# Kernel tuning notes

Hardware: AMD Instinct MI355X
Metric: run time of the kernel (lower is better)

Reference implementation:

```python
import jax, jax.numpy as jnp
import numpy as np
from jax import lax

G = 1000  # hard-coded grid size in ConvCNP.forward
LOG_2PI = float(np.log(2.0 * np.pi))


def _conv1d(x, w, b):
    # x: (B, Cin, L), w: (Cout, Cin, K), SAME padding, stride 1 (k=5, pad=2)
    y = lax.conv_general_dilated(x, w, (1,), 'SAME',
                                 dimension_numbers=('NCH', 'OIH', 'NCH'))
    return y + b[None, :, None]


def setup_inputs() -> dict:
    key = jax.random.key(0)
    ks = jax.random.split(key, 16)
    B, Nc, Nt = 32, 2048, 2048
    inp = {
        'x_context': jax.random.normal(ks[0], (B, 1, Nc), jnp.float32),
        'y_context': jax.random.normal(ks[1], (B, 1, Nc), jnp.float32),
        'x_target': jax.random.normal(ks[2], (B, 1, Nt), jnp.float32),
        'y_target': jax.random.normal(ks[3], (B, 1, Nt), jnp.float32),
        # learned kernel lengthscales (nn.Parameter init 0.5)
        'ls_x': jnp.asarray(0.5, jnp.float32),
        'ls_rho': jnp.asarray(0.5, jnp.float32),
        # SimpleCNN(2, 1): channels [2, 16, 32, 16, 2], k=5
        'W1': 0.1 * jax.random.normal(ks[4], (16, 2, 5), jnp.float32),
        'b1': jnp.zeros((16,), jnp.float32),
        'W2': 0.1 * jax.random.normal(ks[5], (32, 16, 5), jnp.float32),
        'b2': jnp.zeros((32,), jnp.float32),
        'W3': 0.1 * jax.random.normal(ks[6], (16, 32, 5), jnp.float32),
        'b3': jnp.zeros((16,), jnp.float32),
        'W4': 0.1 * jax.random.normal(ks[7], (2, 16, 5), jnp.float32),
        'b4': jnp.zeros((2,), jnp.float32),
    }
    return inp


def _forward(x_context, y_context, x_target, y_target,
             ls_x, ls_rho, W1, b1, W2, b2, W3, b3, W4, b4):
    B = x_context.shape[0]
    xc = x_context[:, 0, :]            # (B, Nc)
    xt = x_target[:, 0, :]             # (B, Nt)
    t = jnp.linspace(-2.2, 2.2, G).astype(x_context.dtype)  # (G,)

    # phi(y) = [1, y] density/signal channels: (B, 2, Nc)
    phi = jnp.concatenate([jnp.ones_like(y_context), y_context], axis=1)

    # EQ-kernel interpolation context -> grid: w[b,g,n] = exp(-(t_g-x_n)^2/(2 l^2))
    d2 = (t[None, :, None] - xc[:, None, :]) ** 2           # (B, G, Nc)
    w_x = jnp.exp(-d2 / (2.0 * ls_x * ls_x))
    h = jnp.einsum('bgn,bcn->bcg', w_x, phi)                # (B, 2, G)

    density = h[:, 0:1, :]
    rest = h[:, 1:, :] / (density + 1e-8)
    h = jnp.concatenate([density, rest], axis=1)            # (B, 2, G)

    # SimpleCNN
    y = jax.nn.relu(_conv1d(h, W1, b1))
    y = jax.nn.relu(_conv1d(y, W2, b2))
    y = jax.nn.relu(_conv1d(y, W3, b3))
    y = _conv1d(y, W4, b4)                                  # (B, 2, G)
    y_mu_grid = y[:, 0:1, :]
    y_sigma_grid = jax.nn.softplus(y[:, 1:2, :])
    y_grid = jnp.concatenate([y_mu_grid, y_sigma_grid], axis=1)  # (B, 2, G)

    # EQ-kernel interpolation grid -> targets
    d2t = (xt[:, :, None] - t[None, None, :]) ** 2          # (B, Nt, G)
    w_rho = jnp.exp(-d2t / (2.0 * ls_rho * ls_rho))
    y_pred = jnp.einsum('btg,bcg->bct', w_rho, y_grid)      # (B, 2, Nt)

    mu = y_pred[:, 0:1, :]
    sigma = y_pred[:, 1:2, :]

    # Normal(mu, sigma).log_prob(y_target), mean over points, sum over batch
    z = (y_target - mu) / sigma
    logp = -0.5 * z * z - jnp.log(sigma) - 0.5 * LOG_2PI    # (B, 1, Nt)
    loss = -jnp.sum(jnp.mean(logp, axis=-1))
    return mu.transpose(0, 2, 1), sigma.transpose(0, 2, 1), loss


def reference(x_context, y_context, x_target, y_target,
              ls_x, ls_rho, W1, b1, W2, b2, W3, b3, W4, b4):
    return _forward(x_context, y_context, x_target, y_target,
                    ls_x, ls_rho, W1, b1, W2, b2, W3, b3, W4, b4)
```

## Files before the change

### kernel.cpp

```cpp
#include <hip/hip_runtime.h>
#include <math.h>

#define G     1000
#define B     32
#define NC    2048
#define NT    2048
#define BN    (B * NT)
#define LOG2E 1.4426950408889634f
#define LN2PI 1.8378770664093453f

#if __has_builtin(__builtin_amdgcn_exp2f)
#define EXP2F(x) __builtin_amdgcn_exp2f(x)
#else
#define EXP2F(x) exp2f(x)
#endif

typedef float f32x2 __attribute__((ext_vector_type(2)));
#define PKFMA(a, b, c) __builtin_elementwise_fma(a, b, c)
#define SPLAT_LO(v)    __builtin_shufflevector(v, v, 0, 0)
#define SPLAT_HI(v)    __builtin_shufflevector(v, v, 1, 1)

__global__ __launch_bounds__(512) void k_smooth(
    const float* __restrict__ xc, const float* __restrict__ yc,
    const float* __restrict__ ls_x, float* __restrict__ h,
    float* __restrict__ loss_slot) {
  __shared__ float2 sxy[NC];
  __shared__ float2 part[8][64];
  if (blockIdx.x == 0 && blockIdx.y == 0 && threadIdx.x == 0) *loss_slot = 0.f;

  int tid = threadIdx.x;
  int b = blockIdx.y, tile = blockIdx.x;
  float ls  = ls_x[0];
  float s   = sqrtf(0.5f * LOG2E) / ls;
  float dlt = s * (4.4f / 999.f);

  const float* xb = xc + b * NC;
  const float* yb = yc + b * NC;
  for (int n = tid; n < NC; n += 512) sxy[n] = make_float2(s * xb[n], yb[n]);
  __syncthreads();

  int lane = tid & 63, w = tid >> 6;
  int ns = lane & 7, gr = lane >> 3;
  int g0 = tile * 64 + gr * 8;
  float v0 = s * -2.2f + dlt * (float)g0;
  float r  = EXP2F(-2.f * dlt * dlt);
  float r3 = r * r * r;
  float r4 = r3 * r;
  const f32x2 R4 = {r4, r4};

  f32x2 h0p[4], h1p[4];
  #pragma unroll
  for (int j = 0; j < 4; ++j) { h0p[j] = (f32x2)0.f; h1p[j] = (f32x2)0.f; }

  const float2* base = sxy + w * 256 + ns;
  #pragma unroll 4
  for (int i = 0; i < 32; ++i) {
    float2 v = base[i * 8];
    float a  = v.x - v0;
    float W0 = EXP2F(64.f - a * a);
    float q  = EXP2F(fmaf(2.f * dlt, a, -dlt * dlt));
    float qq = q * q;
    f32x2 W2 = {W0, W0 * q};
    f32x2 S2 = {qq * r, qq * r3};
    f32x2 y2 = {v.y, v.y};
    #pragma unroll
    for (int j = 0; j < 4; ++j) {
      h0p[j] += W2;
      h1p[j] = PKFMA(W2, y2, h1p[j]);
      W2 *= S2;
      S2 *= R4;
    }
  }
  #pragma unroll
  for (int m = 1; m < 8; m <<= 1) {
    #pragma unroll
    for (int j = 0; j < 4; ++j) {
      h0p[j].x += __shfl_xor(h0p[j].x, m);
      h0p[j].y += __shfl_xor(h0p[j].y, m);
      h1p[j].x += __shfl_xor(h1p[j].x, m);
      h1p[j].y += __shfl_xor(h1p[j].y, m);
    }
  }
  #pragma unroll
  for (int j = 0; j < 4; ++j) {
    if (ns == j) {
      part[w][gr * 8 + 2 * j]     = make_float2(h0p[j].x, h1p[j].x);
      part[w][gr * 8 + 2 * j + 1] = make_float2(h0p[j].y, h1p[j].y);
    }
  }
  __syncthreads();

  if (tid < 64) {
    int g = tile * 64 + tid;
    if (g < G) {
      float d0 = 0.f, d1 = 0.f;
      #pragma unroll
      for (int k = 0; k < 8; ++k) { float2 pv = part[k][tid]; d0 += pv.x; d1 += pv.y; }
      d0 *= 0x1p-64f;
      d1 *= 0x1p-64f;
      h[(b * 2 + 0) * G + g] = d0;
      h[(b * 2 + 1) * G + g] = d1 / (d0 + 1e-8f);
    }
  }
}

#define TILE  48
#define NTILE 21
#define CSTR  68

template <int CIN, int COUT, int S4>
__device__ __forceinline__ void conv8(
    const float* __restrict__ in, float* __restrict__ out,
    const float4* __restrict__ wf4, const float* __restrict__ w4p,
    const float* __restrict__ bias, int tid) {
  if (tid < COUT * 8) {
    int oc = tid % COUT;
    int i0 = (tid / COUT) * 8;
    float acc[8];
    float bb = bias[oc];
    #pragma unroll
    for (int p = 0; p < 8; ++p) acc[p] = bb;
    for (int ic = 0; ic < CIN; ++ic) {
      const float4* ip = (const float4*)(in + ic * CSTR + i0);
      float4 A = ip[0], Bv = ip[1], C = ip[2];
      float v[12] = {A.x, A.y, A.z, A.w, Bv.x, Bv.y, Bv.z, Bv.w, C.x, C.y, C.z, C.w};
      float4 w = wf4[oc * S4 + ic];
      float w4v = w4p[ic * COUT + oc];
      #pragma unroll
      for (int p = 0; p < 8; ++p)
        acc[p] = fmaf(v[p], w.x, fmaf(v[p+1], w.y, fmaf(v[p+2], w.z,
                 fmaf(v[p+3], w.w, fmaf(v[p+4], w4v, acc[p])))));
    }
    float* op = out + oc * CSTR + i0 + 2;
    #pragma unroll
    for (int j = 0; j < 4; ++j)
      *(float2*)(op + 2 * j) = make_float2(fmaxf(acc[2*j], 0.f), fmaxf(acc[2*j+1], 0.f));
  }
}

template <int CIN, int COUT, int S4>
__device__ __forceinline__ void conv4(
    const float* __restrict__ in, float* __restrict__ out,
    const float4* __restrict__ wf4, const float* __restrict__ w4p,
    const float* __restrict__ bias, int tid) {
  int oc = tid % COUT;
  int i0 = (tid / COUT) * 4;
  float acc[4];
  float bb = bias[oc];
  #pragma unroll
  for (int p = 0; p < 4; ++p) acc[p] = bb;
  for (int ic = 0; ic < CIN; ++ic) {
    const float4* ip = (const float4*)(in + ic * CSTR + i0);
    float4 A = ip[0], Bv = ip[1];
    float v[8] = {A.x, A.y, A.z, A.w, Bv.x, Bv.y, Bv.z, Bv.w};
    float4 w = wf4[oc * S4 + ic];
    float w4v = w4p[ic * COUT + oc];
    #pragma unroll
    for (int p = 0; p < 4; ++p)
      acc[p] = fmaf(v[p], w.x, fmaf(v[p+1], w.y, fmaf(v[p+2], w.z,
               fmaf(v[p+3], w.w, fmaf(v[p+4], w4v, acc[p])))));
  }
  float* op = out + oc * CSTR + i0 + 2;
  *(float2*)op       = make_float2(fmaxf(acc[0], 0.f), fmaxf(acc[1], 0.f));
  *(float2*)(op + 2) = make_float2(fmaxf(acc[2], 0.f), fmaxf(acc[3], 0.f));
}

__global__ __launch_bounds__(256, 2) void k_conv(
    const float* __restrict__ h,
    const float* __restrict__ W1, const float* __restrict__ Bs1,
    const float* __restrict__ W2, const float* __restrict__ Bs2,
    const float* __restrict__ W3, const float* __restrict__ Bs3,
    const float* __restrict__ W4, const float* __restrict__ Bs4,
    float* __restrict__ yg) {
  __shared__ __align__(16) float bufA[32 * CSTR], bufB[32 * CSTR];
  __shared__ float4 wf1[16 * 3], wf2[32 * 17], wf3[16 * 33];
  __shared__ float  w41[2 * 16], w42[16 * 32], w43[32 * 16];
  __shared__ float  wt4[162];
  __shared__ float  sB1[16], sB2[32], sB3[16], sB4[2];

  int tid  = threadIdx.x;
  int tile = blockIdx.x, b = blockIdx.y;
  int ts   = tile * TILE;

  if (tid < 32) {
    int oc = tid >> 1, ic = tid & 1, a = oc * 10 + ic * 5;
    wf1[oc * 3 + ic] = make_float4(W1[a], W1[a+1], W1[a+2], W1[a+3]);
    w41[ic * 16 + oc] = W1[a + 4];
  }
  for (int pr = tid; pr < 512; pr += 256) {
    int oc = pr >> 4, ic = pr & 15, a = oc * 80 + ic * 5;
    wf2[oc * 17 + ic] = make_float4(W2[a], W2[a+1], W2[a+2], W2[a+3]);
    w42[ic * 32 + oc] = W2[a + 4];
  }
  for (int pr = tid; pr < 512; pr += 256) {
    int oc = pr >> 5, ic = pr & 31, a = oc * 160 + ic * 5;
    wf3[oc * 33 + ic] = make_float4(W3[a], W3[a+1], W3[a+2], W3[a+3]);
    w43[ic * 16 + oc] = W3[a + 4];
  }
  for (int i = tid; i < 160; i += 256) wt4[(i / 80) * 81 + i % 80] = W4[i];
  if (tid < 16)       sB1[tid]      = Bs1[tid];
  else if (tid < 48)  sB2[tid - 16] = Bs2[tid - 16];
  else if (tid < 64)  sB3[tid - 48] = Bs3[tid - 48];
  else if (tid < 66)  sB4[tid - 64] = Bs4[tid - 64];

  for (int i = tid; i < 2 * CSTR; i += 256) {
    int c = i >= CSTR, col = i - c * CSTR;
    int g = ts + col - 10;
    bufA[c * CSTR + col] = (g >= 0 && g < G) ? h[(b * 2 + c) * G + g] : 0.f;
  }
  __syncthreads();

  conv4<2, 16, 3>(bufA, bufB, wf1, w41, sB1, tid);
  __syncthreads();
  conv8<16, 32, 17>(bufB, bufA, wf2, w42, sB2, tid);
  __syncthreads();
  conv4<32, 16, 33>(bufA, bufB, wf3, w43, sB3, tid);
  __syncthreads();

  if (tid < 96) {
    int oc = tid >= 48;
    int j  = tid - oc * 48;
    int i  = 10 + j;
    float sacc = sB4[oc];
    #pragma unroll
    for (int ic = 0; ic < 16; ++ic) {
      const float* ip = bufB + ic * CSTR + i - 2;
      #pragma unroll
      for (int k = 0; k < 5; ++k)
        sacc = fmaf(ip[k], wt4[oc * 81 + ic * 5 + k], sacc);
    }
    int gp = ts + j;
    if (gp < G) {
      if (oc == 0) {
        yg[(b * 2 + 0) * G + gp] = sacc;
      } else {
        float sp_ = fmaxf(sacc, 0.f) + log1pf(__expf(-fabsf(sacc)));
        yg[(b * 2 + 1) * G + gp] = sp_;
      }
    }
  }
}

__global__ __launch_bounds__(512) void k_pred(
    const float* __restrict__ xt, const float* __restrict__ yt,
    const float* __restrict__ ls_rho, const float* __restrict__ yg,
    float* __restrict__ out) {
  __shared__ float4 sp[512];
  __shared__ float pA0[512], pA1[512], pB0[512], pB1[512];
  __shared__ float red[8];

  int tid = threadIdx.x;
  int b = blockIdx.y, tile = blockIdx.x;
  float ls = ls_rho[0];
  float s  = sqrtf(0.5f * LOG2E) / ls;
  float dl = s * (4.4f / 999.f);

  const float* y0 = yg + (b * 2 + 0) * G;
  const float* y1 = yg + (b * 2 + 1) * G;
  {
    int g0 = 2 * tid, g1 = 2 * tid + 1;
    float a0 = (g0 < G) ? y0[g0] : 0.f, b0_ = (g0 < G) ? y1[g0] : 0.f;
    float a1 = (g1 < G) ? y0[g1] : 0.f, b1_ = (g1 < G) ? y1[g1] : 0.f;
    sp[tid] = make_float4(a0, b0_, a1, b1_);
  }
  __syncthreads();

  int lane = tid & 63, wv = tid >> 6;
  int ta = tile * 128 + lane;
  float ua = s * xt[b * NT + ta];
  float ub = s * xt[b * NT + ta + 64];
  float base = 2.2f * s - dl * (float)(wv * 128);
  float aa = ua + base, ab = ub + base;
  float r = EXP2F(-2.f * dl * dl);
  f32x2 Wab = {EXP2F(64.f - aa * aa), EXP2F(64.f - ab * ab)};
  f32x2 qab = {EXP2F(dl * (aa + aa) - dl * dl), EXP2F(dl * (ab + ab) - dl * dl)};
  const f32x2 R2 = {r, r};

  f32x2 accA = (f32x2)0.f, accB = (f32x2)0.f;
  const float4* p = sp + wv * 64;
  #pragma unroll 4
  for (int i = 0; i < 64; ++i) {
    float4 v = p[i];
    f32x2 v01 = {v.x, v.y};
    f32x2 v23 = {v.z, v.w};
    accA = PKFMA(SPLAT_LO(Wab), v01, accA);
    accB = PKFMA(SPLAT_HI(Wab), v01, accB);
    Wab *= qab; qab *= R2;
    accA = PKFMA(SPLAT_LO(Wab), v23, accA);
    accB = PKFMA(SPLAT_HI(Wab), v23, accB);
    Wab *= qab; qab *= R2;
  }
  pA0[tid] = accA.x; pA1[tid] = accA.y; pB0[tid] = accB.x; pB1[tid] = accB.y;
  __syncthreads();

  float lp = 0.f;
  if (tid < 128) {
    int which = tid >> 6, l = tid & 63;
    int t = tile * 128 + which * 64 + l;
    const float* q0 = which ? pB0 : pA0;
    const float* q1 = which ? pB1 : pA1;
    float mu = 0.f, sg = 0.f;
    #pragma unroll
    for (int k = 0; k < 8; ++k) { mu += q0[l + 64 * k]; sg += q1[l + 64 * k]; }
    mu *= 0x1p-64f;
    sg *= 0x1p-64f;
    out[b * NT + t]      = mu;
    out[BN + b * NT + t] = sg;
    float z = (yt[b * NT + t] - mu) / sg;
    lp = -0.5f * z * z - __logf(sg) - 0.5f * LN2PI;
  }
  #pragma unroll
  for (int m = 32; m; m >>= 1) lp += __shfl_xor(lp, m);
  if ((tid & 63) == 0) red[tid >> 6] = lp;
  __syncthreads();
  if (tid == 0) {
    float tot = 0.f;
    #pragma unroll
    for (int i = 0; i < 8; ++i) tot += red[i];
    atomicAdd(out + 2 * BN, -tot * (1.f / (float)NT));
  }
}

extern "C" void kernel_launch(void* const* d_in, const int* in_sizes, int n_in,
                              void* d_out, int out_size, void* d_ws, size_t ws_size,
                              hipStream_t stream) {
  const float* xc  = (const float*)d_in[0];
  const float* yc  = (const float*)d_in[1];
  const float* xt  = (const float*)d_in[2];
  const float* yt  = (const float*)d_in[3];
  const float* lsx = (const float*)d_in[4];
  const float* lsr = (const float*)d_in[5];
  const float* W1  = (const float*)d_in[6];  const float* b1 = (const float*)d_in[7];
  const float* W2  = (const float*)d_in[8];  const float* b2 = (const float*)d_in[9];
  const float* W3  = (const float*)d_in[10]; const float* b3 = (const float*)d_in[11];
  const float* W4  = (const float*)d_in[12]; const float* b4 = (const float*)d_in[13];

  float* out = (float*)d_out;
  float* h   = (float*)d_ws;
  float* yg  = h + B * 2 * G;

  k_smooth<<<dim3(16, B), 512, 0, stream>>>(xc, yc, lsx, h, out + 2 * BN);
  k_conv<<<dim3(NTILE, B), 256, 0, stream>>>(h, W1, b1, W2, b2, W3, b3, W4, b4, yg);
  k_pred<<<dim3(16, B), 512, 0, stream>>>(xt, yt, lsr, yg, out);
}
```

Baseline: 37.26 us.

## Use packed FP32 FMA over output-channel pairs in conv layers 2 and 3

```diff
diff --git a/kernel.cpp b/kernel.cpp
--- a/kernel.cpp
+++ b/kernel.cpp
@@ -17,8 +17,14 @@
 
 typedef float f32x2 __attribute__((ext_vector_type(2)));
 #define PKFMA(a, b, c) __builtin_elementwise_fma(a, b, c)
+#define PKMAX(a, b)    __builtin_elementwise_max(a, b)
 #define SPLAT_LO(v)    __builtin_shufflevector(v, v, 0, 0)
 #define SPLAT_HI(v)    __builtin_shufflevector(v, v, 1, 1)
+
+static __device__ __forceinline__ f32x2 splat2(float x) {
+  f32x2 r = {x, x};
+  return r;
+}
 
 __global__ __launch_bounds__(512) void k_smooth(
     const float* __restrict__ xc, const float* __restrict__ yc,
@@ -62,7 +68,7 @@
     float qq = q * q;
     f32x2 W2 = {W0, W0 * q};
     f32x2 S2 = {qq * r, qq * r3};
-    f32x2 y2 = {v.y, v.y};
+    f32x2 y2 = splat2(v.y);
     #pragma unroll
     for (int j = 0; j < 4; ++j) {
       h0p[j] += W2;
@@ -108,53 +114,23 @@
 #define NTILE 21
 #define CSTR  68
 
-template <int CIN, int COUT, int S4>
-__device__ __forceinline__ void conv8(
+__device__ __forceinline__ void conv4_l1(
     const float* __restrict__ in, float* __restrict__ out,
     const float4* __restrict__ wf4, const float* __restrict__ w4p,
     const float* __restrict__ bias, int tid) {
-  if (tid < COUT * 8) {
-    int oc = tid % COUT;
-    int i0 = (tid / COUT) * 8;
-    float acc[8];
-    float bb = bias[oc];
-    #pragma unroll
-    for (int p = 0; p < 8; ++p) acc[p] = bb;
-    for (int ic = 0; ic < CIN; ++ic) {
-      const float4* ip = (const float4*)(in + ic * CSTR + i0);
-      float4 A = ip[0], Bv = ip[1], C = ip[2];
-      float v[12] = {A.x, A.y, A.z, A.w, Bv.x, Bv.y, Bv.z, Bv.w, C.x, C.y, C.z, C.w};
-      float4 w = wf4[oc * S4 + ic];
-      float w4v = w4p[ic * COUT + oc];
-      #pragma unroll
-      for (int p = 0; p < 8; ++p)
-        acc[p] = fmaf(v[p], w.x, fmaf(v[p+1], w.y, fmaf(v[p+2], w.z,
-                 fmaf(v[p+3], w.w, fmaf(v[p+4], w4v, acc[p])))));
-    }
-    float* op = out + oc * CSTR + i0 + 2;
-    #pragma unroll
-    for (int j = 0; j < 4; ++j)
-      *(float2*)(op + 2 * j) = make_float2(fmaxf(acc[2*j], 0.f), fmaxf(acc[2*j+1], 0.f));
-  }
-}
-
-template <int CIN, int COUT, int S4>
-__device__ __forceinline__ void conv4(
-    const float* __restrict__ in, float* __restrict__ out,
-    const float4* __restrict__ wf4, const float* __restrict__ w4p,
-    const float* __restrict__ bias, int tid) {
-  int oc = tid % COUT;
-  int i0 = (tid / COUT) * 4;
+  int oc = tid & 15;
+  int i0 = (tid >> 4) * 4;
   float acc[4];
   float bb = bias[oc];
   #pragma unroll
   for (int p = 0; p < 4; ++p) acc[p] = bb;
-  for (int ic = 0; ic < CIN; ++ic) {
+  #pragma unroll
+  for (int ic = 0; ic < 2; ++ic) {
     const float4* ip = (const float4*)(in + ic * CSTR + i0);
     float4 A = ip[0], Bv = ip[1];
     float v[8] = {A.x, A.y, A.z, A.w, Bv.x, Bv.y, Bv.z, Bv.w};
-    float4 w = wf4[oc * S4 + ic];
-    float w4v = w4p[ic * COUT + oc];
+    float4 w = wf4[oc * 3 + ic];
+    float w4v = w4p[ic * 16 + oc];
     #pragma unroll
     for (int p = 0; p < 4; ++p)
       acc[p] = fmaf(v[p], w.x, fmaf(v[p+1], w.y, fmaf(v[p+2], w.z,
@@ -163,6 +139,91 @@
   float* op = out + oc * CSTR + i0 + 2;
   *(float2*)op       = make_float2(fmaxf(acc[0], 0.f), fmaxf(acc[1], 0.f));
   *(float2*)(op + 2) = make_float2(fmaxf(acc[2], 0.f), fmaxf(acc[3], 0.f));
+}
+
+__device__ __forceinline__ void conv_pk_l2(
+    const float* __restrict__ in, float* __restrict__ out,
+    const f32x2* __restrict__ wpk, const float* __restrict__ bias, int tid) {
+  int lane = tid & 63, w = tid >> 6;
+  int pair = lane & 15, subL = lane >> 4;
+  int i0 = (w * 4 + subL) * 4;
+  int oc0 = pair * 2;
+  f32x2 bb = {bias[oc0], bias[oc0 + 1]};
+  f32x2 acc2[4];
+  #pragma unroll
+  for (int p = 0; p < 4; ++p) acc2[p] = bb;
+  #pragma unroll 4
+  for (int ic = 0; ic < 16; ++ic) {
+    const float4* ip = (const float4*)(in + ic * CSTR + i0);
+    float4 A = ip[0], Bv = ip[1];
+    float v[8] = {A.x, A.y, A.z, A.w, Bv.x, Bv.y, Bv.z, Bv.w};
+    const f32x2* wp = wpk + pair * 81 + ic * 5;
+    f32x2 w0 = wp[0], w1 = wp[1], w2 = wp[2], w3 = wp[3], w4 = wp[4];
+    #pragma unroll
+    for (int p = 0; p < 4; ++p) {
+      acc2[p] = PKFMA(w0, splat2(v[p]),   acc2[p]);
+      acc2[p] = PKFMA(w1, splat2(v[p+1]), acc2[p]);
+      acc2[p] = PKFMA(w2, splat2(v[p+2]), acc2[p]);
+      acc2[p] = PKFMA(w3, splat2(v[p+3]), acc2[p]);
+      acc2[p] = PKFMA(w4, splat2(v[p+4]), acc2[p]);
+    }
+  }
+  #pragma unroll
+  for (int p = 0; p < 4; ++p) acc2[p] = PKMAX(acc2[p], (f32x2)0.f);
+  float* o0 = out + oc0 * CSTR + i0 + 2;
+  float* o1 = o0 + CSTR;
+  *(float2*)o0       = make_float2(acc2[0].x, acc2[1].x);
+  *(float2*)(o0 + 2) = make_float2(acc2[2].x, acc2[3].x);
+  *(float2*)o1       = make_float2(acc2[0].y, acc2[1].y);
+  *(float2*)(o1 + 2) = make_float2(acc2[2].y, acc2[3].y);
+}
+
+__device__ __forceinline__ void conv_pk_l3(
+    const float* __restrict__ in, float* __restrict__ out,
+    const f32x2* __restrict__ wpk, const float* __restrict__ bias, int tid) {
+  int lane = tid & 63, w = tid >> 6;
+  int ichalf = lane >> 5;
+  int pair   = (lane >> 2) & 7;
+  int subL   = lane & 3;
+  int i0 = (w * 4 + subL) * 4;
+  int icb = ichalf * 16;
+  f32x2 acc2[4];
+  #pragma unroll
+  for (int p = 0; p < 4; ++p) acc2[p] = (f32x2)0.f;
+  #pragma unroll 4
+  for (int j = 0; j < 16; ++j) {
+    int ic = icb + j;
+    const float4* ip = (const float4*)(in + ic * CSTR + i0);
+    float4 A = ip[0], Bv = ip[1];
+    float v[8] = {A.x, A.y, A.z, A.w, Bv.x, Bv.y, Bv.z, Bv.w};
+    const f32x2* wp = wpk + pair * 161 + ic * 5;
+    f32x2 w0 = wp[0], w1 = wp[1], w2 = wp[2], w3 = wp[3], w4 = wp[4];
+    #pragma unroll
+    for (int p = 0; p < 4; ++p) {
+      acc2[p] = PKFMA(w0, splat2(v[p]),   acc2[p]);
+      acc2[p] = PKFMA(w1, splat2(v[p+1]), acc2[p]);
+      acc2[p] = PKFMA(w2, splat2(v[p+2]), acc2[p]);
+      acc2[p] = PKFMA(w3, splat2(v[p+3]), acc2[p]);
+      acc2[p] = PKFMA(w4, splat2(v[p+4]), acc2[p]);
+    }
+  }
+  #pragma unroll
+  for (int p = 0; p < 4; ++p) {
+    acc2[p].x += __shfl_xor(acc2[p].x, 32);
+    acc2[p].y += __shfl_xor(acc2[p].y, 32);
+  }
+  if (ichalf == 0) {
+    int oc0 = pair * 2;
+    f32x2 bb = {bias[oc0], bias[oc0 + 1]};
+    #pragma unroll
+    for (int p = 0; p < 4; ++p) acc2[p] = PKMAX(acc2[p] + bb, (f32x2)0.f);
+    float* o0 = out + oc0 * CSTR + i0 + 2;
+    float* o1 = o0 + CSTR;
+    *(float2*)o0       = make_float2(acc2[0].x, acc2[1].x);
+    *(float2*)(o0 + 2) = make_float2(acc2[2].x, acc2[3].x);
+    *(float2*)o1       = make_float2(acc2[0].y, acc2[1].y);
+    *(float2*)(o1 + 2) = make_float2(acc2[2].y, acc2[3].y);
+  }
 }
 
 __global__ __launch_bounds__(256, 2) void k_conv(
@@ -173,8 +234,10 @@
     const float* __restrict__ W4, const float* __restrict__ Bs4,
     float* __restrict__ yg) {
   __shared__ __align__(16) float bufA[32 * CSTR], bufB[32 * CSTR];
-  __shared__ float4 wf1[16 * 3], wf2[32 * 17], wf3[16 * 33];
-  __shared__ float  w41[2 * 16], w42[16 * 32], w43[32 * 16];
+  __shared__ float4 wf1[16 * 3];
+  __shared__ float  w41[2 * 16];
+  __shared__ f32x2  wp2[16 * 81];
+  __shared__ f32x2  wp3[8 * 161];
   __shared__ float  wt4[162];
   __shared__ float  sB1[16], sB2[32], sB3[16], sB4[2];
 
@@ -187,15 +250,15 @@
     wf1[oc * 3 + ic] = make_float4(W1[a], W1[a+1], W1[a+2], W1[a+3]);
     w41[ic * 16 + oc] = W1[a + 4];
   }
-  for (int pr = tid; pr < 512; pr += 256) {
-    int oc = pr >> 4, ic = pr & 15, a = oc * 80 + ic * 5;
-    wf2[oc * 17 + ic] = make_float4(W2[a], W2[a+1], W2[a+2], W2[a+3]);
-    w42[ic * 32 + oc] = W2[a + 4];
-  }
-  for (int pr = tid; pr < 512; pr += 256) {
-    int oc = pr >> 5, ic = pr & 31, a = oc * 160 + ic * 5;
-    wf3[oc * 33 + ic] = make_float4(W3[a], W3[a+1], W3[a+2], W3[a+3]);
-    w43[ic * 16 + oc] = W3[a + 4];
+  for (int i = tid; i < 1280; i += 256) {
+    int pair = i / 80, rem = i - pair * 80;
+    f32x2 t = {W2[(2*pair)*80 + rem], W2[(2*pair+1)*80 + rem]};
+    wp2[pair * 81 + rem] = t;
+  }
+  for (int i = tid; i < 1280; i += 256) {
+    int pair = i / 160, rem = i - pair * 160;
+    f32x2 t = {W3[(2*pair)*160 + rem], W3[(2*pair+1)*160 + rem]};
+    wp3[pair * 161 + rem] = t;
   }
   for (int i = tid; i < 160; i += 256) wt4[(i / 80) * 81 + i % 80] = W4[i];
   if (tid < 16)       sB1[tid]      = Bs1[tid];
@@ -210,11 +273,11 @@
   }
   __syncthreads();
 
-  conv4<2, 16, 3>(bufA, bufB, wf1, w41, sB1, tid);
-  __syncthreads();
-  conv8<16, 32, 17>(bufB, bufA, wf2, w42, sB2, tid);
-  __syncthreads();
-  conv4<32, 16, 33>(bufA, bufB, wf3, w43, sB3, tid);
+  conv4_l1(bufA, bufB, wf1, w41, sB1, tid);
+  __syncthreads();
+  conv_pk_l2(bufB, bufA, wp2, sB2, tid);
+  __syncthreads();
+  conv_pk_l3(bufA, bufB, wp3, sB3, tid);
   __syncthreads();
 
   if (tid < 96) {
```

New measurement: 38.90 us. 1.04x slower.
